# Optimization experiments

Measured on AMD Instinct MI355X. Metric: run time of the kernel, lower is better.

## Reference

```python
import jax, jax.numpy as jnp
import numpy as np

N = 8192
IN_F = 128
OUT_F = 64
ALPHA = 0.2  # LeakyReLU negative slope
NEG_BIG = -9e15

def _xavier(key, shape, gain=1.414):
    fan_in, fan_out = shape[0], shape[1]
    limit = gain * np.sqrt(6.0 / (fan_in + fan_out))
    return jax.random.uniform(key, shape, jnp.float32, -limit, limit)

def setup_inputs() -> dict:
    key = jax.random.key(0)
    k1, k2, k3, k4 = jax.random.split(key, 4)
    h = jax.random.normal(k1, (N, IN_F), jnp.float32)
    adj = jax.random.randint(k2, (N, N), 0, 2, jnp.int32)
    W = _xavier(k3, (IN_F, OUT_F))
    a = _xavier(k4, (2 * OUT_F, 1))
    return {"h": h, "adj": adj, "W": W, "a": a}

def reference(h, adj, W, a):
    Wh = h @ W                                  # [N, OUT_F]
    a1 = a[:OUT_F, 0]                           # [OUT_F]
    a2 = a[OUT_F:, 0]                           # [OUT_F]
    e = (Wh @ a1)[:, None] + (Wh @ a2)[None, :] # [N, N] additive score
    e = jnp.where(e > 0, e, ALPHA * e)          # LeakyReLU
    e = jnp.where(adj > 0, e, NEG_BIG)          # mask non-edges
    attention = jax.nn.softmax(e, axis=1)       # [N, N]
    h_prime = attention @ Wh                    # [N, OUT_F]
    return jax.nn.elu(h_prime)                  # concat=True path
```

## Files before the change

### kernel.cpp

```cpp
#include <hip/hip_runtime.h>
#include <hip/hip_bf16.h>
#include <math.h>

#define NN 8192
#define INF_ 128
#define OUTF 64

typedef __attribute__((ext_vector_type(4))) float f32x4;
typedef __attribute__((ext_vector_type(2))) int i32x2;
typedef __attribute__((ext_vector_type(8))) unsigned short u16x8;
typedef __attribute__((ext_vector_type(8))) __bf16 bf16x8;

#define BAR()                                                    \
    {                                                            \
        asm volatile("s_waitcnt lgkmcnt(0)" ::: "memory");       \
        __builtin_amdgcn_s_barrier();                            \
    }

__device__ __forceinline__ unsigned short f2bf(float f) {
    unsigned int u = __float_as_uint(f);
    u = (u + 0x7FFFu + ((u >> 16) & 1u)) >> 16;
    return (unsigned short)u;
}

__global__ __launch_bounds__(256) void prep_kernel(
    const float* __restrict__ h, const float* __restrict__ W,
    const float* __restrict__ a, unsigned short* __restrict__ WhT,
    float* __restrict__ f1, float* __restrict__ f2)
{
    __shared__ float W_lds[INF_ * OUTF];
    __shared__ float h_lds[32 * INF_];
    __shared__ unsigned short t_lds[OUTF * 34];

    const int t = threadIdx.x;
    const int rb = blockIdx.x * 32;

    {
        const float4* Ws = (const float4*)W;
        float4* Wd = (float4*)W_lds;
        #pragma unroll
        for (int q = 0; q < 8; ++q) Wd[t + 256 * q] = Ws[t + 256 * q];
        const float4* hs = (const float4*)(h + (size_t)rb * INF_);
        float4* hd = (float4*)h_lds;
        #pragma unroll
        for (int q = 0; q < 4; ++q) hd[t + 256 * q] = hs[t + 256 * q];
    }
    __syncthreads();

    const int lane = t & 63;
    const int w = t >> 6;

    float acc[8];
    #pragma unroll
    for (int q = 0; q < 8; ++q) acc[q] = 0.f;
    for (int k = 0; k < INF_; ++k) {
        const float wv = W_lds[k * OUTF + lane];
        #pragma unroll
        for (int q = 0; q < 8; ++q)
            acc[q] = fmaf(h_lds[(w * 8 + q) * INF_ + k], wv, acc[q]);
    }

    const float a1 = a[lane];
    const float a2 = a[OUTF + lane];
    #pragma unroll
    for (int q = 0; q < 8; ++q) {
        float s1 = acc[q] * a1;
        float s2 = acc[q] * a2;
        #pragma unroll
        for (int m = 1; m < 64; m <<= 1) {
            s1 += __shfl_xor(s1, m, 64);
            s2 += __shfl_xor(s2, m, 64);
        }
        if (lane == 0) {
            f1[rb + w * 8 + q] = s1;
            f2[rb + w * 8 + q] = s2;
        }
        t_lds[lane * 34 + w * 8 + q] = f2bf(acc[q]);
    }
    __syncthreads();
    {
        const int c = t >> 2;
        const int ro = (t & 3) * 8;
        unsigned int pk[4];
        #pragma unroll
        for (int i = 0; i < 4; ++i) {
            const unsigned int lo = t_lds[c * 34 + ro + 2 * i];
            const unsigned int hi = t_lds[c * 34 + ro + 2 * i + 1];
            pk[i] = lo | (hi << 16);
        }
        *(uint4*)(WhT + (size_t)c * NN + rb + ro) = make_uint4(pk[0], pk[1], pk[2], pk[3]);
    }
}

__global__ __launch_bounds__(1024) void fmax_kernel(
    const float* __restrict__ f2, float* __restrict__ f2max)
{
    __shared__ float red[16];
    const int t = threadIdx.x;
    float m = -INFINITY;
    #pragma unroll
    for (int q = 0; q < NN / 1024; ++q) m = fmaxf(m, f2[t + q * 1024]);
    #pragma unroll
    for (int s = 1; s < 64; s <<= 1) m = fmaxf(m, __shfl_xor(m, s, 64));
    if ((t & 63) == 0) red[t >> 6] = m;
    __syncthreads();
    if (t == 0) {
        float r = red[0];
        #pragma unroll
        for (int i = 1; i < 16; ++i) r = fmaxf(r, red[i]);
        f2max[0] = r;
    }
}

__global__ __launch_bounds__(256) void repack_kernel(
    const unsigned short* __restrict__ WhT, unsigned short* __restrict__ WhTs)
{
    const int ch = blockIdx.x;
    const int t = threadIdx.x;
    const int qd = t >> 6, l = t & 63;
    const int r = l & 15, g = l >> 4;
    const u16x8 v = *(const u16x8*)(WhT + (size_t)(qd * 16 + r) * NN + ch * 32 + g * 8);
    *(u16x8*)(WhTs + (size_t)ch * 2048 + qd * 512 + l * 8) = v;
}

__global__ __launch_bounds__(1024) void bd_kernel(
    const float* __restrict__ f2, unsigned int* __restrict__ bd)
{
    const int i = blockIdx.x * 1024 + threadIdx.x;
    const float v = f2[i];
    const unsigned int B = f2bf(expf(v));
    const unsigned int D = f2bf(expf(0.2f * v));
    bd[i] = B | (D << 16);
}

__global__ __launch_bounds__(512) void gatz_kernel(
    const int* __restrict__ adj, const unsigned short* __restrict__ WhTs,
    const float* __restrict__ f1, const unsigned int* __restrict__ bd,
    const float* __restrict__ f2max, float* __restrict__ out)
{
    __shared__ float acc_lds[8 * 16 * OUTF];
    __shared__ unsigned int bd_lds[NN];
    __shared__ float l_lds[8 * 16];

    const int t = threadIdx.x;
    const int lane = t & 63;
    const int w = t >> 6;
    const int r = lane & 15;
    const int g = lane >> 4;
    const int row_base = blockIdx.x * 16;

    #pragma unroll
    for (int q = 0; q < 4; ++q)
        ((uint4*)bd_lds)[t + 512 * q] = ((const uint4*)bd)[t + 512 * q];

    const float f1r = f1[row_base + r];
    float Mr = f1r + f2max[0];
    Mr = fmaxf(Mr, 0.2f * Mr);
    const float A = expf(f1r - Mr);
    const float C = expf(0.2f * f1r - Mr);
    const unsigned int THb = (unsigned int)f2bf(expf(-f1r));

    f32x4 accl = {0.f, 0.f, 0.f, 0.f};
    f32x4 acc[4];
    #pragma unroll
    for (int q = 0; q < 4; ++q) acc[q] = accl;

    u16x8 ones_u;
    #pragma unroll
    for (int i = 0; i < 8; ++i) ones_u[i] = 0x3F80;
    const bf16x8 bones = __builtin_bit_cast(bf16x8, ones_u);

    const int j0 = w * 1024;
    const int* base = adj + (size_t)row_base * NN + j0 + 2 * lane;
    const u16x8* wv = (const u16x8*)WhTs + lane;

    i32x2 st[16];
    #pragma unroll
    for (int rr = 0; rr < 16; ++rr)
        st[rr] = *(const i32x2*)(base + (size_t)rr * NN);

    BAR();

    for (int s = 0; s < 8; ++s) {
        unsigned long long k0 = 0ull, k1 = 0ull;
        #pragma unroll
        for (int rr = 0; rr < 16; ++rr) {
            const i32x2 v = st[rr];
            const unsigned long long b0 = __ballot(v[0] > 0);
            const unsigned long long b1 = __ballot(v[1] > 0);
            if (rr == r) { k0 = b0; k1 = b1; }
        }
        if (s + 1 < 8) {
            #pragma unroll
            for (int rr = 0; rr < 16; ++rr)
                st[rr] = *(const i32x2*)(base + (size_t)rr * NN + (s + 1) * 128);
        }
        #pragma unroll
        for (int cc = 0; cc < 4; ++cc) {
            const int jl = s * 128 + cc * 32;
            const int col = j0 + jl + g * 8;
            const int ch = (j0 + jl) >> 5;
            const unsigned int sh = 16 * cc + 4 * g;
            const unsigned int m0 = (unsigned int)(k0 >> sh) & 0xFu;
            const unsigned int m1 = (unsigned int)(k1 >> sh) & 0xFu;
            const uint4 bq0 = *(const uint4*)(bd_lds + col);
            const uint4 bq1 = *(const uint4*)(bd_lds + col + 4);
            const unsigned int bdv[8] = {bq0.x, bq0.y, bq0.z, bq0.w,
                                         bq1.x, bq1.y, bq1.z, bq1.w};

            u16x8 pb;
            #pragma unroll
            for (int i = 0; i < 8; ++i) {
                const unsigned int v = bdv[i];
                const unsigned int bb = v & 0xFFFFu;
                const bool up = bb > THb;
                const unsigned int sel = up ? bb : (v >> 16);
                const float f = __uint_as_float(sel << 16);
                const float as = up ? A : C;
                const unsigned int bit = (((i & 1) ? m1 : m0) >> (i >> 1)) & 1u;
                const float p = bit ? f * as : 0.f;
                pb[i] = __builtin_bit_cast(unsigned short, __float2bfloat16(p));
            }

            const bf16x8 af = __builtin_bit_cast(bf16x8, pb);
            #pragma unroll
            for (int qd = 0; qd < 4; ++qd) {
                const bf16x8 bq = __builtin_bit_cast(bf16x8, wv[((size_t)ch * 4 + qd) * 64]);
                acc[qd] = __builtin_amdgcn_mfma_f32_16x16x32_bf16(af, bq, acc[qd], 0, 0, 0);
            }
            accl = __builtin_amdgcn_mfma_f32_16x16x32_bf16(af, bones, accl, 0, 0, 0);
        }
    }

    if (r == 0) {
        #pragma unroll
        for (int q = 0; q < 4; ++q) l_lds[w * 16 + 4 * g + q] = accl[q];
    }
    #pragma unroll
    for (int q = 0; q < 4; ++q) {
        const int m = 4 * g + q;
        #pragma unroll
        for (int qd = 0; qd < 4; ++qd)
            acc_lds[(w * 16 + m) * OUTF + qd * 16 + r] = acc[qd][q];
    }
    __syncthreads();

    {
        #pragma unroll
        for (int hh = 0; hh < 2; ++hh) {
            const int idx = t + hh * 512;
            const int row = idx >> 6;
            const int col = idx & 63;
            float L = 0.f, o = 0.f;
            #pragma unroll
            for (int ww = 0; ww < 8; ++ww) {
                L += l_lds[ww * 16 + row];
                o += acc_lds[(ww * 16 + row) * OUTF + col];
            }
            o /= L;
            o = (o > 0.f) ? o : expm1f(o);
            out[(size_t)(row_base + row) * OUTF + col] = o;
        }
    }
}

extern "C" void kernel_launch(void* const* d_in, const int* in_sizes, int n_in,
                              void* d_out, int out_size, void* d_ws, size_t ws_size,
                              hipStream_t stream) {
    const float* h = (const float*)d_in[0];
    const int* adj = (const int*)d_in[1];
    const float* W = (const float*)d_in[2];
    const float* a = (const float*)d_in[3];
    float* out = (float*)d_out;

    char* ws = (char*)d_ws;
    unsigned short* WhT = (unsigned short*)ws;
    unsigned short* WhTs = (unsigned short*)(ws + (1 << 20));
    float* f1 = (float*)(ws + (2 << 20));
    float* f2 = f1 + NN;
    float* f2m = f2 + NN;
    unsigned int* bd = (unsigned int*)(f2m + 64);

    prep_kernel<<<NN / 32, 256, 0, stream>>>(h, W, a, WhT, f1, f2);
    fmax_kernel<<<1, 1024, 0, stream>>>(f2, f2m);
    bd_kernel<<<NN / 1024, 1024, 0, stream>>>(f2, bd);
    repack_kernel<<<NN / 32, 256, 0, stream>>>(WhT, WhTs);
    gatz_kernel<<<NN / 16, 512, 0, stream>>>(adj, WhTs, f1, bd, f2m, out);
}
```

Measured before the change: 76.77 us.

## Split attention over column blocks with LDS-staged Wh and separate merge kernel

The main kernel now gives each block 128 rows × 512 columns instead of 16 rows × all columns. The 512-column WhT slice and its bd values are staged in LDS and reused by 8 waves, each handling 16 rows, instead of every block reading Wh from global memory. Partial numerators and denominators for the 16 column blocks go to workspace, and a new merge kernel sums them, normalizes and applies ELU. This trades the repeated global Wh reads and the narrow adj loads for extra partial-sum traffic (about 32 MB written and read back) and one more launch.

```diff
diff --git a/kernel.cpp b/kernel.cpp
--- a/kernel.cpp
+++ b/kernel.cpp
@@ -5,9 +5,11 @@
 #define NN 8192
 #define INF_ 128
 #define OUTF 64
+#define RB 128
+#define JB 512
 
 typedef __attribute__((ext_vector_type(4))) float f32x4;
-typedef __attribute__((ext_vector_type(2))) int i32x2;
+typedef __attribute__((ext_vector_type(4))) int i32x4;
 typedef __attribute__((ext_vector_type(8))) unsigned short u16x8;
 typedef __attribute__((ext_vector_type(8))) __bf16 bf16x8;
 
@@ -133,27 +135,38 @@
     bd[i] = B | (D << 16);
 }
 
-__global__ __launch_bounds__(512) void gatz_kernel(
+__global__ __launch_bounds__(512) void gatl_kernel(
     const int* __restrict__ adj, const unsigned short* __restrict__ WhTs,
     const float* __restrict__ f1, const unsigned int* __restrict__ bd,
-    const float* __restrict__ f2max, float* __restrict__ out)
-{
-    __shared__ float acc_lds[8 * 16 * OUTF];
-    __shared__ unsigned int bd_lds[NN];
-    __shared__ float l_lds[8 * 16];
+    const float* __restrict__ f2max, float* __restrict__ pacc,
+    float* __restrict__ pl)
+{
+    __shared__ uint4 whts_lds[4096];
+    __shared__ unsigned int bd_lds[JB];
 
     const int t = threadIdx.x;
     const int lane = t & 63;
     const int w = t >> 6;
     const int r = lane & 15;
     const int g = lane >> 4;
-    const int row_base = blockIdx.x * 16;
-
-    #pragma unroll
-    for (int q = 0; q < 4; ++q)
-        ((uint4*)bd_lds)[t + 512 * q] = ((const uint4*)bd)[t + 512 * q];
-
-    const float f1r = f1[row_base + r];
+    const int rb = (blockIdx.x >> 4) * RB;
+    const int jbi = blockIdx.x & 15;
+    const int jb = jbi * JB;
+
+    const int* base = adj + (size_t)(rb + w * 16) * NN + jb + 4 * lane;
+    i32x4 st[16];
+    #pragma unroll
+    for (int rr = 0; rr < 16; ++rr)
+        st[rr] = *(const i32x4*)(base + (size_t)rr * NN);
+
+    {
+        const uint4* src = (const uint4*)WhTs + (size_t)(jb >> 5) * 256;
+        #pragma unroll
+        for (int q = 0; q < 8; ++q) whts_lds[t + 512 * q] = src[t + 512 * q];
+        if (t < 128) ((uint4*)bd_lds)[t] = ((const uint4*)(bd + jb))[t];
+    }
+
+    const float f1r = f1[rb + w * 16 + r];
     float Mr = f1r + f2max[0];
     Mr = fmaxf(Mr, 0.2f * Mr);
     const float A = expf(f1r - Mr);
@@ -170,41 +183,40 @@
     for (int i = 0; i < 8; ++i) ones_u[i] = 0x3F80;
     const bf16x8 bones = __builtin_bit_cast(bf16x8, ones_u);
 
-    const int j0 = w * 1024;
-    const int* base = adj + (size_t)row_base * NN + j0 + 2 * lane;
-    const u16x8* wv = (const u16x8*)WhTs + lane;
-
-    i32x2 st[16];
-    #pragma unroll
-    for (int rr = 0; rr < 16; ++rr)
-        st[rr] = *(const i32x2*)(base + (size_t)rr * NN);
-
     BAR();
 
-    for (int s = 0; s < 8; ++s) {
-        unsigned long long k0 = 0ull, k1 = 0ull;
+    #pragma unroll
+    for (int s = 0; s < 2; ++s) {
+        unsigned long long km[4];
         #pragma unroll
         for (int rr = 0; rr < 16; ++rr) {
-            const i32x2 v = st[rr];
+            const i32x4 v = st[rr];
             const unsigned long long b0 = __ballot(v[0] > 0);
             const unsigned long long b1 = __ballot(v[1] > 0);
-            if (rr == r) { k0 = b0; k1 = b1; }
-        }
-        if (s + 1 < 8) {
+            const unsigned long long b2 = __ballot(v[2] > 0);
+            const unsigned long long b3 = __ballot(v[3] > 0);
+            if (rr == r) { km[0] = b0; km[1] = b1; km[2] = b2; km[3] = b3; }
+        }
+        if (s + 1 < 2) {
             #pragma unroll
             for (int rr = 0; rr < 16; ++rr)
-                st[rr] = *(const i32x2*)(base + (size_t)rr * NN + (s + 1) * 128);
-        }
-        #pragma unroll
-        for (int cc = 0; cc < 4; ++cc) {
-            const int jl = s * 128 + cc * 32;
-            const int col = j0 + jl + g * 8;
-            const int ch = (j0 + jl) >> 5;
-            const unsigned int sh = 16 * cc + 4 * g;
-            const unsigned int m0 = (unsigned int)(k0 >> sh) & 0xFu;
-            const unsigned int m1 = (unsigned int)(k1 >> sh) & 0xFu;
-            const uint4 bq0 = *(const uint4*)(bd_lds + col);
-            const uint4 bq1 = *(const uint4*)(bd_lds + col + 4);
+                st[rr] = *(const i32x4*)(base + (size_t)rr * NN + 256);
+        }
+        __builtin_amdgcn_sched_barrier(0x38F);
+
+        #pragma unroll
+        for (int cq = 0; cq < 8; ++cq) {
+            const int chl = s * 8 + cq;
+            const int coll = chl * 32 + g * 8;
+            const unsigned int shq = 8 * cq + 2 * g;
+            const unsigned int e0 = (unsigned int)(km[0] >> shq) & 3u;
+            const unsigned int e1 = (unsigned int)(km[1] >> shq) & 3u;
+            const unsigned int e2 = (unsigned int)(km[2] >> shq) & 3u;
+            const unsigned int e3 = (unsigned int)(km[3] >> shq) & 3u;
+            const unsigned int eb[4] = {e0, e1, e2, e3};
+
+            const uint4 bq0 = *(const uint4*)(bd_lds + coll);
+            const uint4 bq1 = *(const uint4*)(bd_lds + coll + 4);
             const unsigned int bdv[8] = {bq0.x, bq0.y, bq0.z, bq0.w,
                                          bq1.x, bq1.y, bq1.z, bq1.w};
 
@@ -217,7 +229,7 @@
                 const unsigned int sel = up ? bb : (v >> 16);
                 const float f = __uint_as_float(sel << 16);
                 const float as = up ? A : C;
-                const unsigned int bit = (((i & 1) ? m1 : m0) >> (i >> 1)) & 1u;
+                const unsigned int bit = (eb[i & 3] >> (i >> 2)) & 1u;
                 const float p = bit ? f * as : 0.f;
                 pb[i] = __builtin_bit_cast(unsigned short, __float2bfloat16(p));
             }
@@ -225,7 +237,8 @@
             const bf16x8 af = __builtin_bit_cast(bf16x8, pb);
             #pragma unroll
             for (int qd = 0; qd < 4; ++qd) {
-                const bf16x8 bq = __builtin_bit_cast(bf16x8, wv[((size_t)ch * 4 + qd) * 64]);
+                const uint4 wqv = whts_lds[chl * 256 + qd * 64 + lane];
+                const bf16x8 bq = __builtin_bit_cast(bf16x8, wqv);
                 acc[qd] = __builtin_amdgcn_mfma_f32_16x16x32_bf16(af, bq, acc[qd], 0, 0, 0);
             }
             accl = __builtin_amdgcn_mfma_f32_16x16x32_bf16(af, bones, accl, 0, 0, 0);
@@ -234,34 +247,35 @@
 
     if (r == 0) {
         #pragma unroll
-        for (int q = 0; q < 4; ++q) l_lds[w * 16 + 4 * g + q] = accl[q];
+        for (int q = 0; q < 4; ++q)
+            pl[(size_t)jbi * NN + rb + w * 16 + 4 * g + q] = accl[q];
     }
     #pragma unroll
     for (int q = 0; q < 4; ++q) {
-        const int m = 4 * g + q;
-        #pragma unroll
-        for (int qd = 0; qd < 4; ++qd)
-            acc_lds[(w * 16 + m) * OUTF + qd * 16 + r] = acc[qd][q];
-    }
-    __syncthreads();
-
-    {
-        #pragma unroll
-        for (int hh = 0; hh < 2; ++hh) {
-            const int idx = t + hh * 512;
-            const int row = idx >> 6;
-            const int col = idx & 63;
-            float L = 0.f, o = 0.f;
-            #pragma unroll
-            for (int ww = 0; ww < 8; ++ww) {
-                L += l_lds[ww * 16 + row];
-                o += acc_lds[(ww * 16 + row) * OUTF + col];
-            }
-            o /= L;
-            o = (o > 0.f) ? o : expm1f(o);
-            out[(size_t)(row_base + row) * OUTF + col] = o;
-        }
-    }
+        const int row = rb + w * 16 + 4 * g + q;
+        float* dst = pacc + ((size_t)jbi * NN + row) * OUTF + r;
+        dst[0]  = acc[0][q];
+        dst[16] = acc[1][q];
+        dst[32] = acc[2][q];
+        dst[48] = acc[3][q];
+    }
+}
+
+__global__ __launch_bounds__(1024) void merge_kernel(
+    const float* __restrict__ pacc, const float* __restrict__ pl,
+    float* __restrict__ out)
+{
+    const size_t idx = (size_t)blockIdx.x * 1024 + threadIdx.x;
+    const int row = (int)(idx >> 6);
+    float L = 0.f, o = 0.f;
+    #pragma unroll
+    for (int k = 0; k < 16; ++k) {
+        L += pl[(size_t)k * NN + row];
+        o += pacc[(size_t)k * NN * OUTF + idx];
+    }
+    o /= L;
+    o = (o > 0.f) ? o : expm1f(o);
+    out[idx] = o;
 }
 
 extern "C" void kernel_launch(void* const* d_in, const int* in_sizes, int n_in,
@@ -279,11 +293,14 @@
     float* f1 = (float*)(ws + (2 << 20));
     float* f2 = f1 + NN;
     float* f2m = f2 + NN;
-    unsigned int* bd = (unsigned int*)(f2m + 64);
+    unsigned int* bd = (unsigned int*)((char*)f2m + 256);
+    float* pacc = (float*)(ws + (4 << 20));
+    float* pl = (float*)(ws + ((size_t)36 << 20));
 
     prep_kernel<<<NN / 32, 256, 0, stream>>>(h, W, a, WhT, f1, f2);
     fmax_kernel<<<1, 1024, 0, stream>>>(f2, f2m);
     bd_kernel<<<NN / 1024, 1024, 0, stream>>>(f2, bd);
     repack_kernel<<<NN / 32, 256, 0, stream>>>(WhT, WhTs);
-    gatz_kernel<<<NN / 16, 512, 0, stream>>>(adj, WhTs, f1, bd, f2m, out);
-}
+    gatl_kernel<<<(NN / RB) * (NN / JB), 512, 0, stream>>>(adj, WhTs, f1, bd, f2m, pacc, pl);
+    merge_kernel<<<NN * OUTF / 1024, 1024, 0, stream>>>(pacc, pl, out);
+}
```

After: 88.14 us. 14.8% more time.

## Split adjacency bit-packing into a separate kernel and consume packed mask in main kernel

Applied to the files above, without the earlier changes.

Adds a bitpack kernel that streams the int32 adjacency matrix once and writes a 1-bit-per-edge mask. The main attention kernel now loads 16 64-bit mask words per lane up front instead of issuing strided int32 loads and 32 ballots per step. WhT fragments are also preloaded per chunk. This decouples the bandwidth-bound adjacency read from the MFMA loop, at the cost of an extra launch and extra global traffic for the bit array.

```diff
diff --git a/kernel.cpp b/kernel.cpp
--- a/kernel.cpp
+++ b/kernel.cpp
@@ -7,7 +7,7 @@
 #define OUTF 64
 
 typedef __attribute__((ext_vector_type(4))) float f32x4;
-typedef __attribute__((ext_vector_type(2))) int i32x2;
+typedef __attribute__((ext_vector_type(4))) int i32x4;
 typedef __attribute__((ext_vector_type(8))) unsigned short u16x8;
 typedef __attribute__((ext_vector_type(8))) __bf16 bf16x8;
 
@@ -133,8 +133,41 @@
     bd[i] = B | (D << 16);
 }
 
-__global__ __launch_bounds__(512) void gatz_kernel(
-    const int* __restrict__ adj, const unsigned short* __restrict__ WhTs,
+__global__ __launch_bounds__(256) void bitpack_kernel(
+    const int* __restrict__ adj, unsigned char* __restrict__ bits)
+{
+    const int row = blockIdx.x;
+    const int t = threadIdx.x;
+    const int lane = t & 63;
+    const int w = t >> 6;
+    const int* src = adj + (size_t)row * NN + w * 2048;
+    unsigned char* dst = bits + (size_t)row * (NN / 8) + w * 256;
+
+    #pragma unroll
+    for (int s = 0; s < 8; ++s) {
+        const i32x4 v = *(const i32x4*)(src + s * 256 + 4 * lane);
+        const unsigned long long b0 = __ballot(v[0] > 0);
+        const unsigned long long b1 = __ballot(v[1] > 0);
+        const unsigned long long b2 = __ballot(v[2] > 0);
+        const unsigned long long b3 = __ballot(v[3] > 0);
+        if (lane < 32) {
+            const unsigned int sh = 2 * lane;
+            unsigned int B =
+                ((unsigned int)(b0 >> sh) & 1u)        |
+                (((unsigned int)(b1 >> sh) & 1u) << 1) |
+                (((unsigned int)(b2 >> sh) & 1u) << 2) |
+                (((unsigned int)(b3 >> sh) & 1u) << 3) |
+                (((unsigned int)(b0 >> (sh + 1)) & 1u) << 4) |
+                (((unsigned int)(b1 >> (sh + 1)) & 1u) << 5) |
+                (((unsigned int)(b2 >> (sh + 1)) & 1u) << 6) |
+                (((unsigned int)(b3 >> (sh + 1)) & 1u) << 7);
+            dst[s * 32 + lane] = (unsigned char)B;
+        }
+    }
+}
+
+__global__ __launch_bounds__(512) void gatb_kernel(
+    const unsigned char* __restrict__ bits, const unsigned short* __restrict__ WhTs,
     const float* __restrict__ f1, const unsigned int* __restrict__ bd,
     const float* __restrict__ f2max, float* __restrict__ out)
 {
@@ -152,6 +185,14 @@
     #pragma unroll
     for (int q = 0; q < 4; ++q)
         ((uint4*)bd_lds)[t + 512 * q] = ((const uint4*)bd)[t + 512 * q];
+
+    unsigned long long km[16];
+    {
+        const unsigned long long* kmp = (const unsigned long long*)
+            (bits + (size_t)(row_base + r) * (NN / 8) + w * 128);
+        #pragma unroll
+        for (int u = 0; u < 16; ++u) km[u] = kmp[u];
+    }
 
     const float f1r = f1[row_base + r];
     float Mr = f1r + f2max[0];
@@ -159,6 +200,7 @@
     const float A = expf(f1r - Mr);
     const float C = expf(0.2f * f1r - Mr);
     const unsigned int THb = (unsigned int)f2bf(expf(-f1r));
+    const unsigned int sh8g = 8u * (unsigned int)g;
 
     f32x4 accl = {0.f, 0.f, 0.f, 0.f};
     f32x4 acc[4];
@@ -170,39 +212,25 @@
     for (int i = 0; i < 8; ++i) ones_u[i] = 0x3F80;
     const bf16x8 bones = __builtin_bit_cast(bf16x8, ones_u);
 
-    const int j0 = w * 1024;
-    const int* base = adj + (size_t)row_base * NN + j0 + 2 * lane;
-    const u16x8* wv = (const u16x8*)WhTs + lane;
-
-    i32x2 st[16];
-    #pragma unroll
-    for (int rr = 0; rr < 16; ++rr)
-        st[rr] = *(const i32x2*)(base + (size_t)rr * NN);
-
     BAR();
 
-    for (int s = 0; s < 8; ++s) {
-        unsigned long long k0 = 0ull, k1 = 0ull;
-        #pragma unroll
-        for (int rr = 0; rr < 16; ++rr) {
-            const i32x2 v = st[rr];
-            const unsigned long long b0 = __ballot(v[0] > 0);
-            const unsigned long long b1 = __ballot(v[1] > 0);
-            if (rr == r) { k0 = b0; k1 = b1; }
-        }
-        if (s + 1 < 8) {
+    {
+        const u16x8* wv = (const u16x8*)WhTs + lane;
+        const int chb = w * 32;
+
+        #pragma unroll
+        for (int cl = 0; cl < 32; ++cl) {
+            const int ch = chb + cl;
+            const int col = ch * 32 + g * 8;
+
+            u16x8 wq[4];
             #pragma unroll
-            for (int rr = 0; rr < 16; ++rr)
-                st[rr] = *(const i32x2*)(base + (size_t)rr * NN + (s + 1) * 128);
-        }
-        #pragma unroll
-        for (int cc = 0; cc < 4; ++cc) {
-            const int jl = s * 128 + cc * 32;
-            const int col = j0 + jl + g * 8;
-            const int ch = (j0 + jl) >> 5;
-            const unsigned int sh = 16 * cc + 4 * g;
-            const unsigned int m0 = (unsigned int)(k0 >> sh) & 0xFu;
-            const unsigned int m1 = (unsigned int)(k1 >> sh) & 0xFu;
+            for (int qd = 0; qd < 4; ++qd)
+                wq[qd] = wv[((size_t)ch * 4 + qd) * 64];
+
+            const unsigned long long kmv = km[cl >> 1];
+            const unsigned int bsh = sh8g + ((cl & 1) << 5);
+
             const uint4 bq0 = *(const uint4*)(bd_lds + col);
             const uint4 bq1 = *(const uint4*)(bd_lds + col + 4);
             const unsigned int bdv[8] = {bq0.x, bq0.y, bq0.z, bq0.w,
@@ -217,7 +245,7 @@
                 const unsigned int sel = up ? bb : (v >> 16);
                 const float f = __uint_as_float(sel << 16);
                 const float as = up ? A : C;
-                const unsigned int bit = (((i & 1) ? m1 : m0) >> (i >> 1)) & 1u;
+                const unsigned int bit = (unsigned int)(kmv >> (bsh + i)) & 1u;
                 const float p = bit ? f * as : 0.f;
                 pb[i] = __builtin_bit_cast(unsigned short, __float2bfloat16(p));
             }
@@ -225,7 +253,7 @@
             const bf16x8 af = __builtin_bit_cast(bf16x8, pb);
             #pragma unroll
             for (int qd = 0; qd < 4; ++qd) {
-                const bf16x8 bq = __builtin_bit_cast(bf16x8, wv[((size_t)ch * 4 + qd) * 64]);
+                const bf16x8 bq = __builtin_bit_cast(bf16x8, wq[qd]);
                 acc[qd] = __builtin_amdgcn_mfma_f32_16x16x32_bf16(af, bq, acc[qd], 0, 0, 0);
             }
             accl = __builtin_amdgcn_mfma_f32_16x16x32_bf16(af, bones, accl, 0, 0, 0);
@@ -279,11 +307,13 @@
     float* f1 = (float*)(ws + (2 << 20));
     float* f2 = f1 + NN;
     float* f2m = f2 + NN;
-    unsigned int* bd = (unsigned int*)(f2m + 64);
+    unsigned int* bd = (unsigned int*)((char*)f2m + 256);
+    unsigned char* bits = (unsigned char*)(ws + (4 << 20));
 
     prep_kernel<<<NN / 32, 256, 0, stream>>>(h, W, a, WhT, f1, f2);
     fmax_kernel<<<1, 1024, 0, stream>>>(f2, f2m);
     bd_kernel<<<NN / 1024, 1024, 0, stream>>>(f2, bd);
     repack_kernel<<<NN / 32, 256, 0, stream>>>(WhT, WhTs);
-    gatz_kernel<<<NN / 16, 512, 0, stream>>>(adj, WhTs, f1, bd, f2m, out);
-}
+    bitpack_kernel<<<NN, 256, 0, stream>>>(adj, bits);
+    gatb_kernel<<<NN / 16, 512, 0, stream>>>(bits, WhTs, f1, bd, f2m, out);
+}
```

Measured after the change: 96.79 us. 1.26x slower.
